# Kernel optimization log

Hardware: AMD Instinct MI355X
Metric: run time of the kernel (lower is better)

Reference implementation:

```python
import jax, jax.numpy as jnp
import numpy as np

BATCH, IN, OUT = 8192, 4096, 4096


def setup_inputs() -> dict:
    key = jax.random.key(0)
    k1, k2, k3 = jax.random.split(key, 3)
    x = jax.random.normal(k1, (BATCH, IN), dtype=jnp.float32)
    weight = jax.random.normal(k2, (OUT, IN), dtype=jnp.float32)
    bias = jax.random.normal(k3, (OUT,), dtype=jnp.float32)
    return {"x": x, "weight": weight, "bias": bias}


def reference(x, weight, bias):
    # Binarize weights/bias with sign (matches torch.sign: sign(0)=0), then fp32 GEMM + bias add.
    w = jnp.sign(weight)            # [OUT, IN], values in {-1, 0, +1}
    b = jnp.sign(bias)              # [OUT]
    return jnp.dot(x, w.T) + b[None, :]   # [BATCH, OUT]
```

## Files before the change

### kernel.cpp

```cpp
#include <hip/hip_runtime.h>
#include <stdint.h>
#include <stddef.h>


#define MDIM 8192
#define NDIM 4096
#define KDIM 4096

typedef __attribute__((ext_vector_type(8))) short bf16x8;
typedef __attribute__((ext_vector_type(4))) float f32x4;

__device__ __forceinline__ short f2bf(float f) {
  union { float f; unsigned u; } a; a.f = f;
  unsigned r = a.u + 0x7FFFu + ((a.u >> 16) & 1u);
  return (short)(r >> 16);
}

__device__ __forceinline__ float fsign(float x) {
  return (x > 0.f) ? 1.f : ((x < 0.f) ? -1.f : 0.f);
}

__device__ __forceinline__ short signbf(float x) {
  return (x > 0.f) ? (short)0x3F80 : ((x < 0.f) ? (short)0xBF80 : (short)0);
}

__device__ __forceinline__ void gl_lds16(const void* g, void* l) {
  __builtin_amdgcn_global_load_lds(
      (const __attribute__((address_space(1))) unsigned*)g,
      (__attribute__((address_space(3))) unsigned*)l,
      16, 0, 0);
}


__global__ void cvt_x_kernel(const float* __restrict__ x, short* __restrict__ o) {
  int i = blockIdx.x * blockDim.x + threadIdx.x;
  float4 v = ((const float4*)x)[i];
  short4 s;
  s.x = f2bf(v.x); s.y = f2bf(v.y); s.z = f2bf(v.z); s.w = f2bf(v.w);
  ((short4*)o)[i] = s;
}

__global__ void cvt_w_kernel(const float* __restrict__ w, short* __restrict__ o) {
  int i = blockIdx.x * blockDim.x + threadIdx.x;
  float4 v = ((const float4*)w)[i];
  short4 s;
  s.x = signbf(v.x); s.y = signbf(v.y); s.z = signbf(v.z); s.w = signbf(v.w);
  ((short4*)o)[i] = s;
}


__global__ __launch_bounds__(256) void gemm_ws(
    const short* __restrict__ A,
    const short* __restrict__ B,
    const float* __restrict__ bias,
    float* __restrict__ C) {
  __shared__ short As[128 * 32];
  __shared__ short Bs[128 * 32];

  const int t    = threadIdx.x;
  const int lane = t & 63;
  const int wm   = (t >> 6) >> 1;
  const int wn   = (t >> 6) & 1;

  const int bm = blockIdx.y * 128;
  const int bn = blockIdx.x * 128;

  f32x4 acc[4][4] = {};

  const int srow = t >> 2;
  const int scol = (t & 3) << 3;

  const short* aA0 = A + (size_t)(bm + srow) * KDIM + scol;
  const short* aA1 = A + (size_t)(bm + 64 + srow) * KDIM + scol;
  const short* aB0 = B + (size_t)(bn + srow) * KDIM + scol;
  const short* aB1 = B + (size_t)(bn + 64 + srow) * KDIM + scol;

  char* ldsA0 = (char*)As + t * 16;
  char* ldsA1 = (char*)As + 4096 + t * 16;
  char* ldsB0 = (char*)Bs + t * 16;
  char* ldsB1 = (char*)Bs + 4096 + t * 16;

  const int fr  = lane & 15;
  const int fkB = (lane >> 4) << 4;

  for (int k0 = 0; k0 < KDIM; k0 += 32) {
    gl_lds16(aA0 + k0, ldsA0);
    gl_lds16(aA1 + k0, ldsA1);
    gl_lds16(aB0 + k0, ldsB0);
    gl_lds16(aB1 + k0, ldsB1);
    __syncthreads();

    bf16x8 af[4], bfr[4];
#pragma unroll
    for (int i = 0; i < 4; ++i) {
      af[i]  = *(const bf16x8*)((const char*)As + (wm * 64 + i * 16 + fr) * 64 + fkB);
      bfr[i] = *(const bf16x8*)((const char*)Bs + (wn * 64 + i * 16 + fr) * 64 + fkB);
    }
#pragma unroll
    for (int i = 0; i < 4; ++i)
#pragma unroll
      for (int j = 0; j < 4; ++j)
        acc[i][j] = __builtin_amdgcn_mfma_f32_16x16x32_bf16(af[i], bfr[j], acc[i][j], 0, 0, 0);
    __syncthreads();
  }

  const int row0 = bm + wm * 64 + ((lane >> 4) << 2);
  const int col0 = bn + wn * 64 + (lane & 15);
#pragma unroll
  for (int j = 0; j < 4; ++j) {
    const int gc = col0 + j * 16;
    const float bs = fsign(bias[gc]);
#pragma unroll
    for (int i = 0; i < 4; ++i) {
      float* cp = C + (size_t)(row0 + i * 16) * NDIM + gc;
#pragma unroll
      for (int r = 0; r < 4; ++r)
        cp[(size_t)r * NDIM] = acc[i][j][r] + bs;
    }
  }
}


__global__ __launch_bounds__(256) void gemm_fused(
    const float* __restrict__ A,
    const float* __restrict__ W,
    const float* __restrict__ bias,
    float* __restrict__ C) {
  __shared__ short As[128 * 32];
  __shared__ short Bs[128 * 32];

  const int t    = threadIdx.x;
  const int lane = t & 63;
  const int wm   = (t >> 6) >> 1;
  const int wn   = (t >> 6) & 1;

  const int bm = blockIdx.y * 128;
  const int bn = blockIdx.x * 128;

  f32x4 acc[4][4] = {};

  const int srow = t >> 1;
  const int scol = (t & 1) << 4;

  const float* pA = A + (size_t)(bm + srow) * KDIM + scol;
  const float* pW = W + (size_t)(bn + srow) * KDIM + scol;
  short* sA = As + srow * 32 + scol;
  short* sB = Bs + srow * 32 + scol;

  const int fr  = lane & 15;
  const int fkB = (lane >> 4) << 4;

  for (int k0 = 0; k0 < KDIM; k0 += 32) {
    float4 va[4], vb[4];
#pragma unroll
    for (int q = 0; q < 4; ++q) {
      va[q] = *(const float4*)(pA + k0 + q * 4);
      vb[q] = *(const float4*)(pW + k0 + q * 4);
    }
    __syncthreads();
    bf16x8 ca, cb;
#pragma unroll
    for (int q = 0; q < 4; ++q) {
      ca[q * 2 + 0] = 0;
    }
    short va_s[16], vb_s[16];
#pragma unroll
    for (int q = 0; q < 4; ++q) {
      va_s[q * 4 + 0] = f2bf(va[q].x); va_s[q * 4 + 1] = f2bf(va[q].y);
      va_s[q * 4 + 2] = f2bf(va[q].z); va_s[q * 4 + 3] = f2bf(va[q].w);
      vb_s[q * 4 + 0] = signbf(vb[q].x); vb_s[q * 4 + 1] = signbf(vb[q].y);
      vb_s[q * 4 + 2] = signbf(vb[q].z); vb_s[q * 4 + 3] = signbf(vb[q].w);
    }
#pragma unroll
    for (int e = 0; e < 8; ++e) { ca[e] = va_s[e]; cb[e] = vb_s[e]; }
    *(bf16x8*)(sA) = ca;
    *(bf16x8*)(sB) = cb;
#pragma unroll
    for (int e = 0; e < 8; ++e) { ca[e] = va_s[8 + e]; cb[e] = vb_s[8 + e]; }
    *(bf16x8*)(sA + 8) = ca;
    *(bf16x8*)(sB + 8) = cb;
    __syncthreads();

    bf16x8 af[4], bfr[4];
#pragma unroll
    for (int i = 0; i < 4; ++i) {
      af[i]  = *(const bf16x8*)((const char*)As + (wm * 64 + i * 16 + fr) * 64 + fkB);
      bfr[i] = *(const bf16x8*)((const char*)Bs + (wn * 64 + i * 16 + fr) * 64 + fkB);
    }
#pragma unroll
    for (int i = 0; i < 4; ++i)
#pragma unroll
      for (int j = 0; j < 4; ++j)
        acc[i][j] = __builtin_amdgcn_mfma_f32_16x16x32_bf16(af[i], bfr[j], acc[i][j], 0, 0, 0);
  }
  __syncthreads();

  const int row0 = bm + wm * 64 + ((lane >> 4) << 2);
  const int col0 = bn + wn * 64 + (lane & 15);
#pragma unroll
  for (int j = 0; j < 4; ++j) {
    const int gc = col0 + j * 16;
    const float bs = fsign(bias[gc]);
#pragma unroll
    for (int i = 0; i < 4; ++i) {
      float* cp = C + (size_t)(row0 + i * 16) * NDIM + gc;
#pragma unroll
      for (int r = 0; r < 4; ++r)
        cp[(size_t)r * NDIM] = acc[i][j][r] + bs;
    }
  }
}

extern "C" void kernel_launch(void* const* d_in, const int* in_sizes, int n_in,
                              void* d_out, int out_size, void* d_ws, size_t ws_size,
                              hipStream_t stream) {
  const float* x    = (const float*)d_in[0];
  const float* w    = (const float*)d_in[1];
  const float* bias = (const float*)d_in[2];
  float* out = (float*)d_out;

  const size_t xb_bytes = (size_t)MDIM * KDIM * 2;
  const size_t wb_bytes = (size_t)NDIM * KDIM * 2;

  dim3 grid(NDIM / 128, MDIM / 128);

  if (ws_size >= xb_bytes + wb_bytes) {
    short* xb = (short*)d_ws;
    short* wb = (short*)((char*)d_ws + xb_bytes);
    cvt_x_kernel<<<(MDIM * (KDIM / 4)) / 256, 256, 0, stream>>>(x, xb);
    cvt_w_kernel<<<(NDIM * (KDIM / 4)) / 256, 256, 0, stream>>>(w, wb);
    gemm_ws<<<grid, 256, 0, stream>>>(xb, wb, bias, out);
  } else {
    gemm_fused<<<grid, 256, 0, stream>>>(x, w, bias, out);
  }
}
```

Baseline: 555.7 us.

## Replace bf16 GEMM with 256x256-tile double-buffered phased MFMA kernel

Replaces the 128x128, single-buffered, two-barrier-per-step GEMM with a 256x256-tile, 512-thread kernel. It uses 128 KB of double-buffered LDS with XOR-swizzled layout and K-step 64. Each iteration is split into four MFMA phases, and the next tile's async global-to-LDS loads are interleaved between them, with explicit waitcnt, barriers and setprio. It also remaps block IDs for L2 locality and uses a larger per-wave register tile to raise reuse. The cost is heavier register use and more complex synchronisation.

After: 478.6 us. -13.9%, faster.

```diff
diff --git a/kernel.cpp b/kernel.cpp
--- a/kernel.cpp
+++ b/kernel.cpp
@@ -6,6 +6,7 @@
 #define MDIM 8192
 #define NDIM 4096
 #define KDIM 4096
+#define NT   (KDIM / 64)
 
 typedef __attribute__((ext_vector_type(8))) short bf16x8;
 typedef __attribute__((ext_vector_type(4))) float f32x4;
@@ -49,73 +50,137 @@
 }
 
 
-__global__ __launch_bounds__(256) void gemm_ws(
+#define STAGE(BUF, HH, KTS) do {                                               \
+    const short* _s = ((HH) < 2 ? aA + (size_t)((HH) * 128) * KDIM             \
+                                : aB + (size_t)(((HH) - 2) * 128) * KDIM)      \
+                      + (size_t)(KTS) * 64;                                    \
+    char* _d = ldst + (BUF) * 65536 + (HH) * 16384;                            \
+    gl_lds16(_s, _d);                                                          \
+    gl_lds16(_s + (size_t)64 * KDIM, _d + 8192);                               \
+  } while (0)
+
+#define READ_A(QOFF) do {                                                      \
+    _Pragma("unroll") for (int i = 0; i < 4; ++i) {                            \
+      const int ro = so + arow + (QOFF) + i * 2048;                            \
+      a[i][0] = *(const bf16x8*)(sm + ro + colp0);                             \
+      a[i][1] = *(const bf16x8*)(sm + ro + colp1);                             \
+    } } while (0)
+
+#define READ_B(DST, QOFF) do {                                                 \
+    _Pragma("unroll") for (int j = 0; j < 2; ++j) {                            \
+      const int ro = so + brow + (QOFF) + j * 2048;                            \
+      DST[j][0] = *(const bf16x8*)(sm + ro + colp0);                           \
+      DST[j][1] = *(const bf16x8*)(sm + ro + colp1);                           \
+    } } while (0)
+
+#define MFMA_Q(I0, J0, BREG) do {                                              \
+    __builtin_amdgcn_s_setprio(1);                                            \
+    _Pragma("unroll") for (int i = 0; i < 4; ++i)                              \
+      _Pragma("unroll") for (int j = 0; j < 2; ++j) {                          \
+        acc[(I0) + i][(J0) + j] = __builtin_amdgcn_mfma_f32_16x16x32_bf16(     \
+            a[i][0], BREG[j][0], acc[(I0) + i][(J0) + j], 0, 0, 0);            \
+        acc[(I0) + i][(J0) + j] = __builtin_amdgcn_mfma_f32_16x16x32_bf16(     \
+            a[i][1], BREG[j][1], acc[(I0) + i][(J0) + j], 0, 0, 0);            \
+      }                                                                        \
+    __builtin_amdgcn_s_setprio(0);                                            \
+  } while (0)
+
+#define SYNC_PRE_MFMA() do {                                                   \
+    __builtin_amdgcn_s_barrier();                                              \
+    asm volatile("s_waitcnt lgkmcnt(0)" ::: "memory");                         \
+    __builtin_amdgcn_sched_barrier(0);                                         \
+  } while (0)
+
+__global__ __launch_bounds__(512, 2) void gemm_8phase(
     const short* __restrict__ A,
     const short* __restrict__ B,
     const float* __restrict__ bias,
     float* __restrict__ C) {
-  __shared__ short As[128 * 32];
-  __shared__ short Bs[128 * 32];
+  __shared__ __align__(16) char sm[131072];
 
   const int t    = threadIdx.x;
   const int lane = t & 63;
-  const int wm   = (t >> 6) >> 1;
-  const int wn   = (t >> 6) & 1;
-
-  const int bm = blockIdx.y * 128;
-  const int bn = blockIdx.x * 128;
-
-  f32x4 acc[4][4] = {};
-
-  const int srow = t >> 2;
-  const int scol = (t & 3) << 3;
-
-  const short* aA0 = A + (size_t)(bm + srow) * KDIM + scol;
-  const short* aA1 = A + (size_t)(bm + 64 + srow) * KDIM + scol;
-  const short* aB0 = B + (size_t)(bn + srow) * KDIM + scol;
-  const short* aB1 = B + (size_t)(bn + 64 + srow) * KDIM + scol;
-
-  char* ldsA0 = (char*)As + t * 16;
-  char* ldsA1 = (char*)As + 4096 + t * 16;
-  char* ldsB0 = (char*)Bs + t * 16;
-  char* ldsB1 = (char*)Bs + 4096 + t * 16;
-
-  const int fr  = lane & 15;
-  const int fkB = (lane >> 4) << 4;
-
-  for (int k0 = 0; k0 < KDIM; k0 += 32) {
-    gl_lds16(aA0 + k0, ldsA0);
-    gl_lds16(aA1 + k0, ldsA1);
-    gl_lds16(aB0 + k0, ldsB0);
-    gl_lds16(aB1 + k0, ldsB1);
-    __syncthreads();
-
-    bf16x8 af[4], bfr[4];
-#pragma unroll
-    for (int i = 0; i < 4; ++i) {
-      af[i]  = *(const bf16x8*)((const char*)As + (wm * 64 + i * 16 + fr) * 64 + fkB);
-      bfr[i] = *(const bf16x8*)((const char*)Bs + (wn * 64 + i * 16 + fr) * 64 + fkB);
-    }
-#pragma unroll
-    for (int i = 0; i < 4; ++i)
-#pragma unroll
-      for (int j = 0; j < 4; ++j)
-        acc[i][j] = __builtin_amdgcn_mfma_f32_16x16x32_bf16(af[i], bfr[j], acc[i][j], 0, 0, 0);
-    __syncthreads();
-  }
-
-  const int row0 = bm + wm * 64 + ((lane >> 4) << 2);
-  const int col0 = bn + wn * 64 + (lane & 15);
-#pragma unroll
-  for (int j = 0; j < 4; ++j) {
-    const int gc = col0 + j * 16;
+  const int w    = t >> 6;
+  const int wm   = w >> 2;
+  const int wn   = w & 3;
+  const int fr   = lane & 15;
+  const int g    = lane >> 4;
+
+  const int bid = blockIdx.y * gridDim.x + blockIdx.x;
+  const int swz = (bid & 7) * 64 + (bid >> 3);
+  const int bm  = (swz >> 4) << 8;
+  const int bn  = (swz & 15) << 8;
+
+  const int sx    = (fr & 7) << 4;
+  const int colp0 = (g << 4) ^ sx;
+  const int colp1 = (64 | (g << 4)) ^ sx;
+  const int arow  = (wm * 128 + fr) * 128;
+  const int brow  = 32768 + (wn * 64 + fr) * 128;
+
+  const int srow = t >> 3;
+  const int scol = ((t & 7) ^ (srow & 7)) << 3;
+  const short* aA = A + (size_t)(bm + srow) * KDIM + scol;
+  const short* aB = B + (size_t)(bn + srow) * KDIM + scol;
+  char* ldst = (char*)sm + t * 16;
+
+  f32x4 acc[8][4] = {};
+  bf16x8 a[4][2], b0[2][2], b1[2][2];
+
+  STAGE(0, 0, 0);
+  STAGE(0, 1, 0);
+  STAGE(0, 2, 0);
+  STAGE(0, 3, 0);
+  STAGE(1, 0, 1);
+  asm volatile("s_waitcnt vmcnt(2)" ::: "memory");
+  __builtin_amdgcn_s_barrier();
+
+  for (int kt = 0; kt < NT; ++kt) {
+    const int so = (kt & 1) << 16;
+    const int nb = (kt & 1) ^ 1;
+    const int cb = (kt & 1);
+
+    READ_A(0);
+    READ_B(b0, 0);
+    if (kt + 1 < NT) STAGE(nb, 1, kt + 1);
+    SYNC_PRE_MFMA();
+    MFMA_Q(0, 0, b0);
+    __builtin_amdgcn_s_barrier();
+
+    READ_B(b1, 4096);
+    if (kt + 1 < NT) STAGE(nb, 2, kt + 1);
+    SYNC_PRE_MFMA();
+    MFMA_Q(0, 2, b1);
+    __builtin_amdgcn_s_barrier();
+
+    READ_A(8192);
+    if (kt + 1 < NT) STAGE(nb, 3, kt + 1);
+    SYNC_PRE_MFMA();
+    MFMA_Q(4, 2, b1);
+    __builtin_amdgcn_s_barrier();
+
+    if (kt + 2 < NT) STAGE(cb, 0, kt + 2);
+    __builtin_amdgcn_s_barrier();
+    MFMA_Q(4, 0, b0);
+    if (kt + 2 < NT) {
+      asm volatile("s_waitcnt vmcnt(2)" ::: "memory");
+    } else {
+      asm volatile("s_waitcnt vmcnt(0)" ::: "memory");
+    }
+    __builtin_amdgcn_s_barrier();
+  }
+
+  const int crow = bm + wm * 128;
+  const int ccol = bn + wn * 64 + fr;
+#pragma unroll
+  for (int jj = 0; jj < 4; ++jj) {
+    const int gc = ccol + jj * 16;
     const float bs = fsign(bias[gc]);
 #pragma unroll
-    for (int i = 0; i < 4; ++i) {
-      float* cp = C + (size_t)(row0 + i * 16) * NDIM + gc;
+    for (int ii = 0; ii < 8; ++ii) {
+      float* cp = C + (size_t)(crow + ii * 16 + g * 4) * NDIM + gc;
 #pragma unroll
       for (int r = 0; r < 4; ++r)
-        cp[(size_t)r * NDIM] = acc[i][j][r] + bs;
+        cp[(size_t)r * NDIM] = acc[ii][jj][r] + bs;
     }
   }
 }
@@ -158,11 +223,6 @@
       vb[q] = *(const float4*)(pW + k0 + q * 4);
     }
     __syncthreads();
-    bf16x8 ca, cb;
-#pragma unroll
-    for (int q = 0; q < 4; ++q) {
-      ca[q * 2 + 0] = 0;
-    }
     short va_s[16], vb_s[16];
 #pragma unroll
     for (int q = 0; q < 4; ++q) {
@@ -171,14 +231,15 @@
       vb_s[q * 4 + 0] = signbf(vb[q].x); vb_s[q * 4 + 1] = signbf(vb[q].y);
       vb_s[q * 4 + 2] = signbf(vb[q].z); vb_s[q * 4 + 3] = signbf(vb[q].w);
     }
-#pragma unroll
-    for (int e = 0; e < 8; ++e) { ca[e] = va_s[e]; cb[e] = vb_s[e]; }
+    bf16x8 ca, cbv;
+#pragma unroll
+    for (int e = 0; e < 8; ++e) { ca[e] = va_s[e]; cbv[e] = vb_s[e]; }
     *(bf16x8*)(sA) = ca;
-    *(bf16x8*)(sB) = cb;
-#pragma unroll
-    for (int e = 0; e < 8; ++e) { ca[e] = va_s[8 + e]; cb[e] = vb_s[8 + e]; }
+    *(bf16x8*)(sB) = cbv;
+#pragma unroll
+    for (int e = 0; e < 8; ++e) { ca[e] = va_s[8 + e]; cbv[e] = vb_s[8 + e]; }
     *(bf16x8*)(sA + 8) = ca;
-    *(bf16x8*)(sB + 8) = cb;
+    *(bf16x8*)(sB + 8) = cbv;
     __syncthreads();
 
     bf16x8 af[4], bfr[4];
@@ -222,15 +283,15 @@
   const size_t xb_bytes = (size_t)MDIM * KDIM * 2;
   const size_t wb_bytes = (size_t)NDIM * KDIM * 2;
 
-  dim3 grid(NDIM / 128, MDIM / 128);
-
   if (ws_size >= xb_bytes + wb_bytes) {
     short* xb = (short*)d_ws;
     short* wb = (short*)((char*)d_ws + xb_bytes);
     cvt_x_kernel<<<(MDIM * (KDIM / 4)) / 256, 256, 0, stream>>>(x, xb);
     cvt_w_kernel<<<(NDIM * (KDIM / 4)) / 256, 256, 0, stream>>>(w, wb);
-    gemm_ws<<<grid, 256, 0, stream>>>(xb, wb, bias, out);
+    dim3 grid(NDIM / 256, MDIM / 256);
+    gemm_8phase<<<grid, 512, 0, stream>>>(xb, wb, bias, out);
   } else {
+    dim3 grid(NDIM / 128, MDIM / 128);
     gemm_fused<<<grid, 256, 0, stream>>>(x, w, bias, out);
   }
 }
```
